# Performance work log

Measured on AMD Instinct MI355X. Metric: run time of the kernel, lower is better.

The kernel has to match this reference:

```python
import jax, jax.numpy as jnp
import numpy as np
from jax.scipy.special import logsumexp

SEQ, BATCH, NUM_TAGS = 1024, 512, 64


def setup_inputs() -> dict:
    key = jax.random.key(0)
    k_em, k_tag, k_len, k_s, k_e, k_t = jax.random.split(key, 6)
    emissions = jax.random.normal(k_em, (SEQ, BATCH, NUM_TAGS), dtype=jnp.float32)
    tags = jax.random.randint(k_tag, (SEQ, BATCH), 0, NUM_TAGS, dtype=jnp.int64)
    # random sequence lengths in [1, SEQ]; mask[0] is guaranteed all ones
    lengths = jax.random.randint(k_len, (BATCH,), 1, SEQ + 1)
    mask = (jnp.arange(SEQ)[:, None] < lengths[None, :]).astype(jnp.int32)
    # CRF params: uniform(-0.1, 0.1) as in reset_parameters()
    u = lambda k, shape: jax.random.uniform(k, shape, jnp.float32, -0.1, 0.1)
    return {
        "emissions": emissions,
        "tags": tags,
        "mask": mask,
        "start_transitions": u(k_s, (NUM_TAGS,)),
        "end_transitions": u(k_e, (NUM_TAGS,)),
        "transitions": u(k_t, (NUM_TAGS, NUM_TAGS)),
    }


def _compute_score(emissions, tags, maskf, start_transitions, end_transitions, transitions):
    # emissions: (S,B,T), tags/maskf: (S,B)
    S, B = tags.shape
    em_scores = jnp.take_along_axis(emissions, tags[:, :, None], axis=2)[..., 0]  # (S,B)
    trans_scores = transitions[tags[:-1], tags[1:]]  # (S-1,B)
    score = start_transitions[tags[0]] + em_scores[0]
    score = score + jnp.sum((trans_scores + em_scores[1:]) * maskf[1:], axis=0)
    seq_ends = maskf.astype(jnp.int32).sum(axis=0) - 1  # (B,)
    last_tags = tags[seq_ends, jnp.arange(B)]
    return score + end_transitions[last_tags]


def _compute_normalizer(emissions, mask, start_transitions, end_transitions, transitions):
    # forward algorithm: sequential logsumexp scan over timesteps
    def step(score, x):  # score: (B,T)
        em_t, m_t = x  # (B,T), (B,)
        nxt = logsumexp(score[:, :, None] + transitions[None, :, :] + em_t[:, None, :], axis=1)
        score = jnp.where(m_t[:, None] > 0, nxt, score)
        return score, None

    score0 = start_transitions[None, :] + emissions[0]  # (B,T)
    score, _ = jax.lax.scan(step, score0, (emissions[1:], mask[1:]))
    return logsumexp(score + end_transitions[None, :], axis=1)  # (B,)


def reference(emissions, tags, mask, start_transitions, end_transitions, transitions):
    maskf = mask.astype(emissions.dtype)
    numerator = _compute_score(emissions, tags, maskf, start_transitions, end_transitions, transitions)
    denominator = _compute_normalizer(emissions, mask, start_transitions, end_transitions, transitions)
    llh = numerator - denominator
    return llh.sum()  # reduction='sum' (default)
```

## Files before the change

### kernel.cpp

```cpp
#include <hip/hip_runtime.h>

#define SEQ 1024
#define BATCH 512
#define NTAGS 64
#define HALF_T 512
#define LOGD 4.158883083f

typedef _Float16 v2h __attribute__((ext_vector_type(2)));

#define FENCE() asm volatile("" ::: "memory")

__device__ __forceinline__ float dot2acc(v2h a, v2h b, float c) {
#if __has_builtin(__builtin_amdgcn_fdot2)
    return __builtin_amdgcn_fdot2(a, b, c, false);
#else
    return fmaf((float)a.x, (float)b.x, fmaf((float)a.y, (float)b.y, c));
#endif
}

__device__ __forceinline__ float rfl(float x) {
    return __uint_as_float(__builtin_amdgcn_readfirstlane(__float_as_uint(x)));
}

__global__ __launch_bounds__(64)
void scan_kernel(const float* __restrict__ em,
                 const int* __restrict__ mask,
                 const float* __restrict__ startT,
                 const float* __restrict__ endT,
                 const float* __restrict__ trans,
                 float* __restrict__ beta_f, float* __restrict__ Mf,
                 float* __restrict__ gma,    float* __restrict__ Mb,
                 int* __restrict__ Lw)
{
    const bool fwd = blockIdx.x < BATCH;
    const int  b   = fwd ? blockIdx.x : blockIdx.x - BATCH;
    const int  j   = threadIdx.x;

    __shared__ __align__(16) _Float16 bsh[NTAGS];

    int lsum = 0;
#pragma unroll
    for (int k = 0; k < SEQ / 64; ++k)
        lsum += mask[(k * 64 + j) * BATCH + b];
#pragma unroll
    for (int off = 32; off > 0; off >>= 1)
        lsum += __shfl_xor(lsum, off);
    const int L = lsum;

    v2h w[32];
#pragma unroll
    for (int i = 0; i < 32; ++i) {
        float a0, a1;
        if (fwd) { a0 = trans[(2 * i) * NTAGS + j]; a1 = trans[(2 * i + 1) * NTAGS + j]; }
        else     { a0 = trans[j * NTAGS + 2 * i];   a1 = trans[j * NTAGS + 2 * i + 1];   }
        v2h t; t.x = (_Float16)__expf(a0); t.y = (_Float16)__expf(a1);
        w[i] = t;
    }

    const float4* bv = (const float4*)bsh;

#define DOT(WRVAL, SOUT)                                                   \
    {                                                                      \
        FENCE();                                                           \
        bsh[j] = (_Float16)(WRVAL);                                        \
        FENCE();                                                           \
        float s0 = 0.f, s1 = 0.f, s2 = 0.f, s3 = 0.f;                      \
        _Pragma("unroll")                                                  \
        for (int q4 = 0; q4 < 8; ++q4) {                                   \
            float4 q = bv[q4];                                             \
            s0 = dot2acc(__builtin_bit_cast(v2h, q.x), w[4 * q4 + 0], s0); \
            s1 = dot2acc(__builtin_bit_cast(v2h, q.y), w[4 * q4 + 1], s1); \
            s2 = dot2acc(__builtin_bit_cast(v2h, q.z), w[4 * q4 + 2], s2); \
            s3 = dot2acc(__builtin_bit_cast(v2h, q.w), w[4 * q4 + 3], s3); \
        }                                                                  \
        SOUT = (s0 + s1) + (s2 + s3);                                      \
    }

    float beta, M;
    int nsteps = 0;

    if (fwd) {
        float em0 = em[(size_t)b * NTAGS + j];
        float a0  = startT[j] + em0;
        M    = __shfl(a0, 0);
        beta = __expf(a0 - M);

        const int Lf = min(L - 1, HALF_T - 1);
        int t = 1;
        float cur[4], nxt[4];
#pragma unroll
        for (int u = 0; u < 4; ++u) {
            cur[u] = em[((size_t)min(t + u,     SEQ - 1) * BATCH + b) * NTAGS + j];
            nxt[u] = em[((size_t)min(t + 4 + u, SEQ - 1) * BATCH + b) * NTAGS + j];
        }
        while (t + 3 <= Lf) {
            float pre[4];
#pragma unroll
            for (int u = 0; u < 4; ++u)
                pre[u] = em[((size_t)min(t + 8 + u, SEQ - 1) * BATCH + b) * NTAGS + j];
            float eem[4];
#pragma unroll
            for (int u = 0; u < 4; ++u) eem[u] = __expf(cur[u] - LOGD);

            float s;
            DOT(beta, s); beta = s * eem[0];
            DOT(beta, s);
            float r = rfl(s);
            beta = s * eem[1];
            DOT(beta, s); beta = s * eem[2];
            float rinv = 1.0f / r;
            float lr   = __logf(r);
            DOT(beta, s); beta = s * (eem[3] * rinv);
            M += lr;
            nsteps += 4;
#pragma unroll
            for (int u = 0; u < 4; ++u) { cur[u] = nxt[u]; nxt[u] = pre[u]; }
            t += 4;
        }
        for (; t <= Lf; ++t) {
            float emt = em[((size_t)t * BATCH + b) * NTAGS + j];
            float s; DOT(beta, s);
            beta = s * __expf(emt - LOGD);
            ++nsteps;
        }

        beta_f[b * NTAGS + j] = beta;
        if (j == 0) {
            Mf[b] = fmaf((float)nsteps, LOGD, M);
            Lw[b] = L;
        }
    } else {
        beta = __expf(endT[j]);
        M = 0.0f;
        if (L - 1 >= HALF_T) {
            int tt = L - 1;
            float cur[4], nxt[4];
#pragma unroll
            for (int u = 0; u < 4; ++u) {
                cur[u] = em[((size_t)max(tt - u,     0) * BATCH + b) * NTAGS + j];
                nxt[u] = em[((size_t)max(tt - 4 - u, 0) * BATCH + b) * NTAGS + j];
            }
            while (tt - 3 >= HALF_T) {
                float pre[4];
#pragma unroll
                for (int u = 0; u < 4; ++u)
                    pre[u] = em[((size_t)max(tt - 8 - u, 0) * BATCH + b) * NTAGS + j];
                float eem[4];
#pragma unroll
                for (int u = 0; u < 4; ++u) eem[u] = __expf(cur[u] - LOGD);

                float s;
                DOT(beta * eem[0], s); beta = s;
                DOT(beta * eem[1], s);
                float r = rfl(s);
                beta = s;
                DOT(beta * eem[2], s); beta = s;
                float rinv = 1.0f / r;
                float lr   = __logf(r);
                DOT(beta * (eem[3] * rinv), s); beta = s;
                M += lr;
                nsteps += 4;
#pragma unroll
                for (int u = 0; u < 4; ++u) { cur[u] = nxt[u]; nxt[u] = pre[u]; }
                tt -= 4;
            }
            for (; tt >= HALF_T; --tt) {
                float emt = em[((size_t)tt * BATCH + b) * NTAGS + j];
                float s; DOT(beta * __expf(emt - LOGD), s);
                beta = s;
                ++nsteps;
            }
        }
        gma[b * NTAGS + j] = beta;
        if (j == 0)
            Mb[b] = fmaf((float)nsteps, LOGD, M);
    }
#undef DOT
}

__global__ __launch_bounds__(64)
void join_kernel(const float* __restrict__ em,
                 const int* __restrict__ tags,
                 const float* __restrict__ startT,
                 const float* __restrict__ endT,
                 const float* __restrict__ trans,
                 const float* __restrict__ beta_f, const float* __restrict__ Mf,
                 const float* __restrict__ gma,    const float* __restrict__ Mb,
                 const int* __restrict__ Lw,
                 float* __restrict__ out)
{
    const int b = blockIdx.x;
    const int j = threadIdx.x;

    __shared__ float tr_sh[NTAGS * NTAGS];
#pragma unroll
    for (int i = 0; i < NTAGS; ++i)
        tr_sh[i * NTAGS + j] = trans[i * NTAGS + j];
    __syncthreads();

    const int L = Lw[b];

    float np = 0.0f;
#pragma unroll
    for (int k = 0; k < SEQ / 64; ++k) {
        int t = k * 64 + j;
        if (t >= 1 && t < L) {
            int ct = tags[t * BATCH + b];
            int pt = tags[(t - 1) * BATCH + b];
            np += tr_sh[pt * NTAGS + ct] + em[((size_t)t * BATCH + b) * NTAGS + ct];
        }
    }
    if (j == 0) {
        int t0 = tags[b];
        np += startT[t0] + em[(size_t)b * NTAGS + t0]
            + endT[tags[(size_t)(L - 1) * BATCH + b]];
    }

    float p = beta_f[b * NTAGS + j] * gma[b * NTAGS + j];

#pragma unroll
    for (int off = 32; off > 0; off >>= 1) {
        np += __shfl_xor(np, off);
        p  += __shfl_xor(p,  off);
    }

    if (j == 0) {
        float denom = __logf(p) + Mf[b] + Mb[b];
        atomicAdd(out, np - denom);
    }
}

extern "C" void kernel_launch(void* const* d_in, const int* in_sizes, int n_in,
                              void* d_out, int out_size, void* d_ws, size_t ws_size,
                              hipStream_t stream)
{
    const float* em     = (const float*)d_in[0];
    const int*   tags   = (const int*)d_in[1];
    const int*   mask   = (const int*)d_in[2];
    const float* startT = (const float*)d_in[3];
    const float* endT   = (const float*)d_in[4];
    const float* trans  = (const float*)d_in[5];
    float*       out    = (float*)d_out;

    float* beta_f = (float*)d_ws;
    float* Mf     = beta_f + BATCH * NTAGS;
    float* gma    = Mf + BATCH;
    float* Mb     = gma + BATCH * NTAGS;
    int*   Lw     = (int*)(Mb + BATCH);

    hipMemsetAsync(out, 0, sizeof(float) * out_size, stream);
    scan_kernel<<<2 * BATCH, 64, 0, stream>>>(em, mask, startT, endT, trans,
                                              beta_f, Mf, gma, Mb, Lw);
    join_kernel<<<BATCH, 64, 0, stream>>>(em, tags, startT, endT, trans,
                                          beta_f, Mf, gma, Mb, Lw, out);
}
```

Measured before the change: 276.8 us.

## Fuse forward/backward scan and join into one kernel with asm LDS dot

Merges the scan and join kernels into a single 128-thread block per batch element, where wave 0 runs the forward half and wave 1 the backward half, and the two combine through shared memory. This removes the second launch and the workspace round trip. The per-step LDS broadcast and dot product become inline assembly with split waitcnts, so the first half of the dot products can start while the remaining reads are still in flight. The risks are halving the block count, which lowers the number of independent waves, and relying on hand-written asm ordering with no explicit barrier between the LDS write and the reads.

Measured after the change: 308.4 us. 1.11x slower.

```diff
diff --git a/kernel.cpp b/kernel.cpp
--- a/kernel.cpp
+++ b/kernel.cpp
@@ -1,4 +1,5 @@
 #include <hip/hip_runtime.h>
+#include <stdint.h>
 
 #define SEQ 1024
 #define BATCH 512
@@ -6,9 +7,8 @@
 #define HALF_T 512
 #define LOGD 4.158883083f
 
-typedef _Float16 v2h __attribute__((ext_vector_type(2)));
-
-#define FENCE() asm volatile("" ::: "memory")
+typedef _Float16 v2h   __attribute__((ext_vector_type(2)));
+typedef float    f32x4 __attribute__((ext_vector_type(4)));
 
 __device__ __forceinline__ float dot2acc(v2h a, v2h b, float c) {
 #if __has_builtin(__builtin_amdgcn_fdot2)
@@ -22,21 +22,29 @@
     return __uint_as_float(__builtin_amdgcn_readfirstlane(__float_as_uint(x)));
 }
 
-__global__ __launch_bounds__(64)
-void scan_kernel(const float* __restrict__ em,
-                 const int* __restrict__ mask,
-                 const float* __restrict__ startT,
-                 const float* __restrict__ endT,
-                 const float* __restrict__ trans,
-                 float* __restrict__ beta_f, float* __restrict__ Mf,
-                 float* __restrict__ gma,    float* __restrict__ Mb,
-                 int* __restrict__ Lw)
+__device__ __forceinline__ v2h bch(float f) { return __builtin_bit_cast(v2h, f); }
+
+__global__ __launch_bounds__(128)
+void crf_kernel(const float* __restrict__ em,
+                const int* __restrict__ tags,
+                const int* __restrict__ mask,
+                const float* __restrict__ startT,
+                const float* __restrict__ endT,
+                const float* __restrict__ trans,
+                float* __restrict__ out)
 {
-    const bool fwd = blockIdx.x < BATCH;
-    const int  b   = fwd ? blockIdx.x : blockIdx.x - BATCH;
-    const int  j   = threadIdx.x;
-
-    __shared__ __align__(16) _Float16 bsh[NTAGS];
+    const int  b   = blockIdx.x;
+    const int  wid = threadIdx.x >> 6;
+    const int  j   = threadIdx.x & 63;
+    const bool fwd = (wid == 0);
+
+    __shared__ __align__(16) _Float16 bsh[2][NTAGS];
+    __shared__ float gsh[NTAGS];
+    __shared__ float mb_np[2];
+
+    const unsigned lbase = (unsigned)(uintptr_t)(&bsh[wid][0]);
+    const unsigned wa    = lbase + 2u * (unsigned)j;
+    const unsigned ra    = lbase;
 
     int lsum = 0;
 #pragma unroll
@@ -57,23 +65,65 @@
         w[i] = t;
     }
 
-    const float4* bv = (const float4*)bsh;
-
-#define DOT(WRVAL, SOUT)                                                   \
-    {                                                                      \
-        FENCE();                                                           \
-        bsh[j] = (_Float16)(WRVAL);                                        \
-        FENCE();                                                           \
-        float s0 = 0.f, s1 = 0.f, s2 = 0.f, s3 = 0.f;                      \
-        _Pragma("unroll")                                                  \
-        for (int q4 = 0; q4 < 8; ++q4) {                                   \
-            float4 q = bv[q4];                                             \
-            s0 = dot2acc(__builtin_bit_cast(v2h, q.x), w[4 * q4 + 0], s0); \
-            s1 = dot2acc(__builtin_bit_cast(v2h, q.y), w[4 * q4 + 1], s1); \
-            s2 = dot2acc(__builtin_bit_cast(v2h, q.z), w[4 * q4 + 2], s2); \
-            s3 = dot2acc(__builtin_bit_cast(v2h, q.w), w[4 * q4 + 3], s3); \
-        }                                                                  \
-        SOUT = (s0 + s1) + (s2 + s3);                                      \
+#define DOT(WRVAL, SOUT)                                                         \
+    {                                                                            \
+        f32x4 q0, q1, q2, q3, q4, q5, q6, q7;                                    \
+        float vtmp;                                                              \
+        asm volatile(                                                            \
+            "v_cvt_f16_f32 %[t], %[v]\n\t"                                       \
+            "ds_write_b16 %[wa], %[t]\n\t"                                       \
+            "ds_read_b128 %[a0], %[ra] offset:0\n\t"                             \
+            "ds_read_b128 %[a1], %[ra] offset:16\n\t"                            \
+            "ds_read_b128 %[a2], %[ra] offset:32\n\t"                            \
+            "ds_read_b128 %[a3], %[ra] offset:48\n\t"                            \
+            "ds_read_b128 %[a4], %[ra] offset:64\n\t"                            \
+            "ds_read_b128 %[a5], %[ra] offset:80\n\t"                            \
+            "ds_read_b128 %[a6], %[ra] offset:96\n\t"                            \
+            "ds_read_b128 %[a7], %[ra] offset:112\n\t"                           \
+            "s_waitcnt lgkmcnt(4)"                                               \
+            : [a0] "=&v"(q0), [a1] "=&v"(q1), [a2] "=&v"(q2), [a3] "=&v"(q3),    \
+              [a4] "=&v"(q4), [a5] "=&v"(q5), [a6] "=&v"(q6), [a7] "=&v"(q7),    \
+              [t] "=&v"(vtmp)                                                    \
+            : [v] "v"(WRVAL), [wa] "v"(wa), [ra] "v"(ra));                       \
+        __builtin_amdgcn_sched_barrier(0);                                       \
+        float s0 = 0.f, s1 = 0.f, s2 = 0.f, s3 = 0.f;                            \
+        s0 = dot2acc(bch(q0.x), w[0],  s0);                                      \
+        s1 = dot2acc(bch(q1.x), w[4],  s1);                                      \
+        s2 = dot2acc(bch(q2.x), w[8],  s2);                                      \
+        s3 = dot2acc(bch(q3.x), w[12], s3);                                      \
+        s0 = dot2acc(bch(q0.y), w[1],  s0);                                      \
+        s1 = dot2acc(bch(q1.y), w[5],  s1);                                      \
+        s2 = dot2acc(bch(q2.y), w[9],  s2);                                      \
+        s3 = dot2acc(bch(q3.y), w[13], s3);                                      \
+        s0 = dot2acc(bch(q0.z), w[2],  s0);                                      \
+        s1 = dot2acc(bch(q1.z), w[6],  s1);                                      \
+        s2 = dot2acc(bch(q2.z), w[10], s2);                                      \
+        s3 = dot2acc(bch(q3.z), w[14], s3);                                      \
+        s0 = dot2acc(bch(q0.w), w[3],  s0);                                      \
+        s1 = dot2acc(bch(q1.w), w[7],  s1);                                      \
+        s2 = dot2acc(bch(q2.w), w[11], s2);                                      \
+        s3 = dot2acc(bch(q3.w), w[15], s3);                                      \
+        asm volatile("s_waitcnt lgkmcnt(0)"                                      \
+                     : "+v"(q4), "+v"(q5), "+v"(q6), "+v"(q7));                  \
+        __builtin_amdgcn_sched_barrier(0);                                       \
+        float s4 = 0.f, s5 = 0.f, s6 = 0.f, s7 = 0.f;                            \
+        s4 = dot2acc(bch(q4.x), w[16], s4);                                      \
+        s5 = dot2acc(bch(q5.x), w[20], s5);                                      \
+        s6 = dot2acc(bch(q6.x), w[24], s6);                                      \
+        s7 = dot2acc(bch(q7.x), w[28], s7);                                      \
+        s4 = dot2acc(bch(q4.y), w[17], s4);                                      \
+        s5 = dot2acc(bch(q5.y), w[21], s5);                                      \
+        s6 = dot2acc(bch(q6.y), w[25], s6);                                      \
+        s7 = dot2acc(bch(q7.y), w[29], s7);                                      \
+        s4 = dot2acc(bch(q4.z), w[18], s4);                                      \
+        s5 = dot2acc(bch(q5.z), w[22], s5);                                      \
+        s6 = dot2acc(bch(q6.z), w[26], s6);                                      \
+        s7 = dot2acc(bch(q7.z), w[30], s7);                                      \
+        s4 = dot2acc(bch(q4.w), w[19], s4);                                      \
+        s5 = dot2acc(bch(q5.w), w[23], s5);                                      \
+        s6 = dot2acc(bch(q6.w), w[27], s6);                                      \
+        s7 = dot2acc(bch(q7.w), w[31], s7);                                      \
+        SOUT = ((s0 + s1) + (s2 + s3)) + ((s4 + s5) + (s6 + s7));                \
     }
 
     float beta, M;
@@ -123,12 +173,6 @@
             beta = s * __expf(emt - LOGD);
             ++nsteps;
         }
-
-        beta_f[b * NTAGS + j] = beta;
-        if (j == 0) {
-            Mf[b] = fmaf((float)nsteps, LOGD, M);
-            Lw[b] = L;
-        }
     } else {
         beta = __expf(endT[j]);
         M = 0.0f;
@@ -171,62 +215,47 @@
                 ++nsteps;
             }
         }
-        gma[b * NTAGS + j] = beta;
-        if (j == 0)
-            Mb[b] = fmaf((float)nsteps, LOGD, M);
     }
 #undef DOT
-}
-
-__global__ __launch_bounds__(64)
-void join_kernel(const float* __restrict__ em,
-                 const int* __restrict__ tags,
-                 const float* __restrict__ startT,
-                 const float* __restrict__ endT,
-                 const float* __restrict__ trans,
-                 const float* __restrict__ beta_f, const float* __restrict__ Mf,
-                 const float* __restrict__ gma,    const float* __restrict__ Mb,
-                 const int* __restrict__ Lw,
-                 float* __restrict__ out)
-{
-    const int b = blockIdx.x;
-    const int j = threadIdx.x;
-
-    __shared__ float tr_sh[NTAGS * NTAGS];
-#pragma unroll
-    for (int i = 0; i < NTAGS; ++i)
-        tr_sh[i * NTAGS + j] = trans[i * NTAGS + j];
-    __syncthreads();
-
-    const int L = Lw[b];
+
+    const float Mfb = fmaf((float)nsteps, LOGD, M);
+
+    if (!fwd) {
+        gsh[j] = beta;
+        if (j == 0) mb_np[0] = Mfb;
+    }
 
     float np = 0.0f;
 #pragma unroll
-    for (int k = 0; k < SEQ / 64; ++k) {
-        int t = k * 64 + j;
+    for (int k = 0; k < SEQ / 128; ++k) {
+        int t = k * 128 + wid * 64 + j;
         if (t >= 1 && t < L) {
             int ct = tags[t * BATCH + b];
             int pt = tags[(t - 1) * BATCH + b];
-            np += tr_sh[pt * NTAGS + ct] + em[((size_t)t * BATCH + b) * NTAGS + ct];
-        }
-    }
-    if (j == 0) {
+            np += trans[pt * NTAGS + ct] + em[((size_t)t * BATCH + b) * NTAGS + ct];
+        }
+    }
+    if (threadIdx.x == 0) {
         int t0 = tags[b];
         np += startT[t0] + em[(size_t)b * NTAGS + t0]
             + endT[tags[(size_t)(L - 1) * BATCH + b]];
     }
-
-    float p = beta_f[b * NTAGS + j] * gma[b * NTAGS + j];
-
-#pragma unroll
-    for (int off = 32; off > 0; off >>= 1) {
+#pragma unroll
+    for (int off = 32; off > 0; off >>= 1)
         np += __shfl_xor(np, off);
-        p  += __shfl_xor(p,  off);
-    }
-
-    if (j == 0) {
-        float denom = __logf(p) + Mf[b] + Mb[b];
-        atomicAdd(out, np - denom);
+    if (!fwd && j == 0) mb_np[1] = np;
+
+    __syncthreads();
+
+    if (fwd) {
+        float p = beta * gsh[j];
+#pragma unroll
+        for (int off = 32; off > 0; off >>= 1)
+            p += __shfl_xor(p, off);
+        if (j == 0) {
+            float denom = __logf(p) + Mfb + mb_np[0];
+            atomicAdd(out, (np + mb_np[1]) - denom);
+        }
     }
 }
 
@@ -242,15 +271,8 @@
     const float* trans  = (const float*)d_in[5];
     float*       out    = (float*)d_out;
 
-    float* beta_f = (float*)d_ws;
-    float* Mf     = beta_f + BATCH * NTAGS;
-    float* gma    = Mf + BATCH;
-    float* Mb     = gma + BATCH * NTAGS;
-    int*   Lw     = (int*)(Mb + BATCH);
+    (void)d_ws; (void)ws_size;
 
     hipMemsetAsync(out, 0, sizeof(float) * out_size, stream);
-    scan_kernel<<<2 * BATCH, 64, 0, stream>>>(em, mask, startT, endT, trans,
-                                              beta_f, Mf, gma, Mb, Lw);
-    join_kernel<<<BATCH, 64, 0, stream>>>(em, tags, startT, endT, trans,
-                                          beta_f, Mf, gma, Mb, Lw, out);
-}
+    crf_kernel<<<BATCH, 128, 0, stream>>>(em, tags, mask, startT, endT, trans, out);
+}
```

## Batch 16 sequences per wave and run CRF forward recursion on MFMA

Applied to the files above, without the earlier changes.

The forward/backward scan now gives each wave 16 batch sequences instead of one. The per-step 64x64 transition product runs as f16 MFMA 16x16x32 instructions, replacing the LDS write/read plus per-lane dot2 loop. Emissions are loaded as f32x4 and prefetched two iterations ahead. Inactive steps are handled with a mask select over a fixed 512-step loop, with renormalization once every four steps. The aim is to cut the per-step latency of the serial chain, at the cost of launching only 64 waves and always running all steps even for short sequences.

Measured after the change: 741.4 us. +167.8%, slower.

```diff
diff --git a/kernel.cpp b/kernel.cpp
--- a/kernel.cpp
+++ b/kernel.cpp
@@ -3,26 +3,42 @@
 #define SEQ 1024
 #define BATCH 512
 #define NTAGS 64
-#define HALF_T 512
 #define LOGD 4.158883083f
 
-typedef _Float16 v2h __attribute__((ext_vector_type(2)));
-
-#define FENCE() asm volatile("" ::: "memory")
-
-__device__ __forceinline__ float dot2acc(v2h a, v2h b, float c) {
-#if __has_builtin(__builtin_amdgcn_fdot2)
-    return __builtin_amdgcn_fdot2(a, b, c, false);
+typedef _Float16 v2h  __attribute__((ext_vector_type(2)));
+typedef _Float16 v8h  __attribute__((ext_vector_type(8)));
+typedef float    f32x4 __attribute__((ext_vector_type(4)));
+typedef unsigned uv4  __attribute__((ext_vector_type(4)));
+
+__device__ __forceinline__ void swap32pair(unsigned x, unsigned& a, unsigned& b) {
+#if __has_builtin(__builtin_amdgcn_permlane32_swap)
+    auto r = __builtin_amdgcn_permlane32_swap(x, x, false, false);
+    a = (unsigned)r[0]; b = (unsigned)r[1];
 #else
-    return fmaf((float)a.x, (float)b.x, fmaf((float)a.y, (float)b.y, c));
+    a = x; b = (unsigned)__shfl_xor((int)x, 32);
 #endif
 }
 
-__device__ __forceinline__ float rfl(float x) {
-    return __uint_as_float(__builtin_amdgcn_readfirstlane(__float_as_uint(x)));
-}
-
-__global__ __launch_bounds__(64)
+__device__ __forceinline__ void swap16pair(unsigned x, unsigned& a, unsigned& b) {
+#if __has_builtin(__builtin_amdgcn_permlane16_swap)
+    auto r = __builtin_amdgcn_permlane16_swap(x, x, false, false);
+    a = (unsigned)r[0]; b = (unsigned)r[1];
+#else
+    a = x; b = (unsigned)__shfl_xor((int)x, 16);
+#endif
+}
+
+__device__ __forceinline__ unsigned pkrtz(float lo, float hi) {
+#if __has_builtin(__builtin_amdgcn_cvt_pkrtz)
+    auto p = __builtin_amdgcn_cvt_pkrtz(lo, hi);
+    return __builtin_bit_cast(unsigned, p);
+#else
+    v2h t; t.x = (_Float16)lo; t.y = (_Float16)hi;
+    return __builtin_bit_cast(unsigned, t);
+#endif
+}
+
+__global__ __launch_bounds__(64, 1)
 void scan_kernel(const float* __restrict__ em,
                  const int* __restrict__ mask,
                  const float* __restrict__ startT,
@@ -32,150 +48,173 @@
                  float* __restrict__ gma,    float* __restrict__ Mb,
                  int* __restrict__ Lw)
 {
-    const bool fwd = blockIdx.x < BATCH;
-    const int  b   = fwd ? blockIdx.x : blockIdx.x - BATCH;
-    const int  j   = threadIdx.x;
-
-    __shared__ __align__(16) _Float16 bsh[NTAGS];
-
-    int lsum = 0;
-#pragma unroll
-    for (int k = 0; k < SEQ / 64; ++k)
-        lsum += mask[(k * 64 + j) * BATCH + b];
-#pragma unroll
-    for (int off = 32; off > 0; off >>= 1)
-        lsum += __shfl_xor(lsum, off);
-    const int L = lsum;
-
-    v2h w[32];
-#pragma unroll
-    for (int i = 0; i < 32; ++i) {
-        float a0, a1;
-        if (fwd) { a0 = trans[(2 * i) * NTAGS + j]; a1 = trans[(2 * i + 1) * NTAGS + j]; }
-        else     { a0 = trans[j * NTAGS + 2 * i];   a1 = trans[j * NTAGS + 2 * i + 1];   }
-        v2h t; t.x = (_Float16)__expf(a0); t.y = (_Float16)__expf(a1);
-        w[i] = t;
-    }
-
-    const float4* bv = (const float4*)bsh;
-
-#define DOT(WRVAL, SOUT)                                                   \
-    {                                                                      \
-        FENCE();                                                           \
-        bsh[j] = (_Float16)(WRVAL);                                        \
-        FENCE();                                                           \
-        float s0 = 0.f, s1 = 0.f, s2 = 0.f, s3 = 0.f;                      \
-        _Pragma("unroll")                                                  \
-        for (int q4 = 0; q4 < 8; ++q4) {                                   \
-            float4 q = bv[q4];                                             \
-            s0 = dot2acc(__builtin_bit_cast(v2h, q.x), w[4 * q4 + 0], s0); \
-            s1 = dot2acc(__builtin_bit_cast(v2h, q.y), w[4 * q4 + 1], s1); \
-            s2 = dot2acc(__builtin_bit_cast(v2h, q.z), w[4 * q4 + 2], s2); \
-            s3 = dot2acc(__builtin_bit_cast(v2h, q.w), w[4 * q4 + 3], s3); \
-        }                                                                  \
-        SOUT = (s0 + s1) + (s2 + s3);                                      \
-    }
-
-    float beta, M;
-    int nsteps = 0;
-
-    if (fwd) {
-        float em0 = em[(size_t)b * NTAGS + j];
-        float a0  = startT[j] + em0;
-        M    = __shfl(a0, 0);
-        beta = __expf(a0 - M);
-
-        const int Lf = min(L - 1, HALF_T - 1);
-        int t = 1;
-        float cur[4], nxt[4];
+    const int  blk = blockIdx.x;
+    const bool isF = blk < (BATCH / 16);
+    const int  b0  = (isF ? blk : blk - BATCH / 16) * 16;
+    const int  l   = threadIdx.x;
+    const int  c   = l & 15;
+    const int  g   = l >> 4;
+
+    int ls = 0;
+#pragma unroll 8
+    for (int i = 0; i < 256; ++i)
+        ls += mask[(g * 256 + i) * BATCH + b0 + c];
+    {
+        unsigned a, b;
+        swap16pair((unsigned)ls, a, b); ls = (int)(a + b);
+        swap32pair((unsigned)ls, a, b); ls = (int)(a + b);
+    }
+    const int Lc   = ls;
+    const int Lact = isF ? min(Lc - 1, 511) : (Lc - 1);
+
+    v8h Af[4][2];
+#pragma unroll
+    for (int m = 0; m < 4; ++m) {
+#pragma unroll
+        for (int kt = 0; kt < 2; ++kt) {
+            v8h a;
+#pragma unroll
+            for (int e = 0; e < 8; ++e) {
+                int srow = (2 * kt + (e >> 2)) * 16 + 4 * g + (e & 3);
+                int orow = m * 16 + c;
+                float tv = isF ? trans[srow * NTAGS + orow]
+                               : trans[orow * NTAGS + srow];
+                a[e] = (_Float16)__expf(tv);
+            }
+            Af[m][kt] = a;
+        }
+    }
+
+    f32x4 P[4];
+    float M;
+    if (isF) {
+        float m0 = startT[0] + em[(size_t)(b0 + c) * NTAGS];
+#pragma unroll
+        for (int m = 0; m < 4; ++m) {
+            f32x4 p;
+#pragma unroll
+            for (int r = 0; r < 4; ++r) {
+                int row = m * 16 + 4 * g + r;
+                p[r] = __expf(startT[row] + em[(size_t)(b0 + c) * NTAGS + row] - m0);
+            }
+            P[m] = p;
+        }
+        M = m0;
+    } else {
+#pragma unroll
+        for (int m = 0; m < 4; ++m) {
+            f32x4 p;
+#pragma unroll
+            for (int r = 0; r < 4; ++r) {
+                int row = m * 16 + 4 * g + r;
+                p[r] = __expf(endT[row]);
+            }
+            P[m] = p;
+        }
+        M = 0.0f;
+    }
+
+#define TSTEP(IT, U) (isF ? (4 * (IT) + (U) + 1) : (1023 - (4 * (IT) + (U))))
+#define EM_LD(T, MM) (*reinterpret_cast<const f32x4*>( \
+        &em[((size_t)(T) * BATCH + b0 + c) * NTAGS + (MM) * 16 + 4 * g]))
+
+    f32x4 curE[4][4], nxtE[4][4];
+#pragma unroll
+    for (int u = 0; u < 4; ++u)
+#pragma unroll
+        for (int m = 0; m < 4; ++m) {
+            curE[u][m] = EM_LD(TSTEP(0, u), m);
+            nxtE[u][m] = EM_LD(TSTEP(1, u), m);
+        }
+
+    const f32x4 z4 = {0.f, 0.f, 0.f, 0.f};
+
+    for (int it = 0; it < 128; ++it) {
 #pragma unroll
         for (int u = 0; u < 4; ++u) {
-            cur[u] = em[((size_t)min(t + u,     SEQ - 1) * BATCH + b) * NTAGS + j];
-            nxt[u] = em[((size_t)min(t + 4 + u, SEQ - 1) * BATCH + b) * NTAGS + j];
-        }
-        while (t + 3 <= Lf) {
-            float pre[4];
-#pragma unroll
-            for (int u = 0; u < 4; ++u)
-                pre[u] = em[((size_t)min(t + 8 + u, SEQ - 1) * BATCH + b) * NTAGS + j];
-            float eem[4];
-#pragma unroll
-            for (int u = 0; u < 4; ++u) eem[u] = __expf(cur[u] - LOGD);
-
-            float s;
-            DOT(beta, s); beta = s * eem[0];
-            DOT(beta, s);
-            float r = rfl(s);
-            beta = s * eem[1];
-            DOT(beta, s); beta = s * eem[2];
-            float rinv = 1.0f / r;
-            float lr   = __logf(r);
-            DOT(beta, s); beta = s * (eem[3] * rinv);
-            M += lr;
-            nsteps += 4;
-#pragma unroll
-            for (int u = 0; u < 4; ++u) { cur[u] = nxt[u]; nxt[u] = pre[u]; }
-            t += 4;
-        }
-        for (; t <= Lf; ++t) {
-            float emt = em[((size_t)t * BATCH + b) * NTAGS + j];
-            float s; DOT(beta, s);
-            beta = s * __expf(emt - LOGD);
-            ++nsteps;
-        }
-
-        beta_f[b * NTAGS + j] = beta;
-        if (j == 0) {
-            Mf[b] = fmaf((float)nsteps, LOGD, M);
-            Lw[b] = L;
+            const int  t   = TSTEP(it, u);
+            const bool act = (t <= Lact);
+
+            f32x4 e4[4];
+#pragma unroll
+            for (int m = 0; m < 4; ++m) {
+                f32x4 x = curE[u][m], y;
+#pragma unroll
+                for (int r = 0; r < 4; ++r) y[r] = __expf(x[r] - LOGD);
+                e4[m] = y;
+            }
+
+            f32x4 T4[4];
+#pragma unroll
+            for (int m = 0; m < 4; ++m)
+                T4[m] = isF ? P[m] : (P[m] * e4[m]);
+
+            unsigned pk0[4], pk1[4];
+#pragma unroll
+            for (int m = 0; m < 4; ++m) {
+                pk0[m] = pkrtz(T4[m][0], T4[m][1]);
+                pk1[m] = pkrtz(T4[m][2], T4[m][3]);
+            }
+            uv4 bw0 = {pk0[0], pk1[0], pk0[1], pk1[1]};
+            uv4 bw1 = {pk0[2], pk1[2], pk0[3], pk1[3]};
+            v8h B0 = __builtin_bit_cast(v8h, bw0);
+            v8h B1 = __builtin_bit_cast(v8h, bw1);
+
+#pragma unroll
+            for (int m = 0; m < 4; ++m) {
+                f32x4 d = __builtin_amdgcn_mfma_f32_16x16x32_f16(Af[m][0], B0, z4, 0, 0, 0);
+                d = __builtin_amdgcn_mfma_f32_16x16x32_f16(Af[m][1], B1, d, 0, 0, 0);
+                f32x4 pn;
+#pragma unroll
+                for (int r = 0; r < 4; ++r)
+                    pn[r] = isF ? (d[r] * e4[m][r]) : d[r];
+#pragma unroll
+                for (int r = 0; r < 4; ++r)
+                    P[m][r] = act ? pn[r] : P[m][r];
+            }
+        }
+
+        {
+            unsigned a, b;
+            float v = P[0][0];
+            swap16pair(__float_as_uint(v), a, b);
+            float s1 = __uint_as_float(a) + __uint_as_float(b);
+            swap32pair(__float_as_uint(s1), a, b);
+            float rr = (__uint_as_float(a) + __uint_as_float(b)) * 16.0f;
+            float ri = 1.0f / rr;
+            M += __logf(rr);
+#pragma unroll
+            for (int m = 0; m < 4; ++m) P[m] *= ri;
+        }
+
+#pragma unroll
+        for (int u = 0; u < 4; ++u)
+#pragma unroll
+            for (int m = 0; m < 4; ++m) {
+                curE[u][m] = nxtE[u][m];
+                nxtE[u][m] = EM_LD(TSTEP(it + 2, u), m);
+            }
+    }
+#undef TSTEP
+#undef EM_LD
+
+    if (isF) {
+#pragma unroll
+        for (int m = 0; m < 4; ++m)
+            *reinterpret_cast<f32x4*>(&beta_f[(size_t)(b0 + c) * NTAGS + m * 16 + 4 * g]) = P[m];
+        if (g == 0) {
+            Mf[b0 + c] = fmaf((float)Lact, LOGD, M);
+            Lw[b0 + c] = Lc;
         }
     } else {
-        beta = __expf(endT[j]);
-        M = 0.0f;
-        if (L - 1 >= HALF_T) {
-            int tt = L - 1;
-            float cur[4], nxt[4];
-#pragma unroll
-            for (int u = 0; u < 4; ++u) {
-                cur[u] = em[((size_t)max(tt - u,     0) * BATCH + b) * NTAGS + j];
-                nxt[u] = em[((size_t)max(tt - 4 - u, 0) * BATCH + b) * NTAGS + j];
-            }
-            while (tt - 3 >= HALF_T) {
-                float pre[4];
-#pragma unroll
-                for (int u = 0; u < 4; ++u)
-                    pre[u] = em[((size_t)max(tt - 8 - u, 0) * BATCH + b) * NTAGS + j];
-                float eem[4];
-#pragma unroll
-                for (int u = 0; u < 4; ++u) eem[u] = __expf(cur[u] - LOGD);
-
-                float s;
-                DOT(beta * eem[0], s); beta = s;
-                DOT(beta * eem[1], s);
-                float r = rfl(s);
-                beta = s;
-                DOT(beta * eem[2], s); beta = s;
-                float rinv = 1.0f / r;
-                float lr   = __logf(r);
-                DOT(beta * (eem[3] * rinv), s); beta = s;
-                M += lr;
-                nsteps += 4;
-#pragma unroll
-                for (int u = 0; u < 4; ++u) { cur[u] = nxt[u]; nxt[u] = pre[u]; }
-                tt -= 4;
-            }
-            for (; tt >= HALF_T; --tt) {
-                float emt = em[((size_t)tt * BATCH + b) * NTAGS + j];
-                float s; DOT(beta * __expf(emt - LOGD), s);
-                beta = s;
-                ++nsteps;
-            }
-        }
-        gma[b * NTAGS + j] = beta;
-        if (j == 0)
-            Mb[b] = fmaf((float)nsteps, LOGD, M);
-    }
-#undef DOT
+#pragma unroll
+        for (int m = 0; m < 4; ++m)
+            *reinterpret_cast<f32x4*>(&gma[(size_t)(b0 + c) * NTAGS + m * 16 + 4 * g]) = P[m];
+        if (g == 0) {
+            int nb = max(Lc - 512, 0);
+            Mb[b0 + c] = fmaf((float)nb, LOGD, M);
+        }
+    }
 }
 
 __global__ __launch_bounds__(64)
@@ -249,8 +288,8 @@
     int*   Lw     = (int*)(Mb + BATCH);
 
     hipMemsetAsync(out, 0, sizeof(float) * out_size, stream);
-    scan_kernel<<<2 * BATCH, 64, 0, stream>>>(em, mask, startT, endT, trans,
-                                              beta_f, Mf, gma, Mb, Lw);
+    scan_kernel<<<2 * (BATCH / 16), 64, 0, stream>>>(em, mask, startT, endT, trans,
+                                                     beta_f, Mf, gma, Mb, Lw);
     join_kernel<<<BATCH, 64, 0, stream>>>(em, tags, startT, endT, trans,
                                           beta_f, Mf, gma, Mb, Lw, out);
 }
```
